# Kernel optimization log

Hardware: AMD Instinct MI355X
Metric: run time of the kernel (lower is better)

The kernel has to match this reference:

```python
import jax, jax.numpy as jnp
import numpy as np

B, T, U = 4, 200, 100
ENC_DIM = 512
PRED_DIM = 512
JOINT_DIM = 640
VOCAB = 1024


def setup_inputs() -> dict:
    key = jax.random.key(0)
    k = jax.random.split(key, 5)
    return {
        "enc_out": jax.random.normal(k[0], (B, T, ENC_DIM), dtype=jnp.float32),
        "pred_out": jax.random.normal(k[1], (B, U, PRED_DIM), dtype=jnp.float32),
        "W_enc": jax.random.normal(k[2], (ENC_DIM, JOINT_DIM), dtype=jnp.float32) / np.sqrt(ENC_DIM),
        "b_enc": jnp.zeros((JOINT_DIM,), dtype=jnp.float32),
        "W_pred": jax.random.normal(k[3], (PRED_DIM, JOINT_DIM), dtype=jnp.float32) / np.sqrt(PRED_DIM),
        "W_out": jax.random.normal(k[4], (JOINT_DIM, VOCAB), dtype=jnp.float32) / np.sqrt(JOINT_DIM),
        "b_out": jnp.zeros((VOCAB,), dtype=jnp.float32),
    }


def reference(enc_out, pred_out, W_enc, b_enc, W_pred, W_out, b_out):
    # Project encoder and prediction-net outputs to joint_dim.
    enc = jnp.einsum("bte,ej->btj", enc_out, W_enc) + b_enc      # [B,T,J]
    pred = jnp.einsum("bup,pj->buj", pred_out, W_pred)           # [B,U,J] (no bias)
    # Broadcast add -> tanh -> vocab projection.
    joint = jnp.tanh(enc[:, :, None, :] + pred[:, None, :, :])   # [B,T,U,J]
    logits = jnp.einsum("btuj,jv->btuv", joint, W_out) + b_out   # [B,T,U,V]
    return logits
```

## Files before the change

kernel.cpp:

```cpp
#include <hip/hip_runtime.h>
#include <hip/hip_bf16.h>

#define B_ 4
#define T_ 200
#define U_ 100
#define ENC_DIM 512
#define JDIM 640
#define VOCAB 1024
#define M_TOTAL (B_*T_*U_)

typedef __attribute__((ext_vector_type(8))) short short8;
typedef __attribute__((ext_vector_type(4))) float float4v;
typedef __attribute__((ext_vector_type(4))) unsigned short ushort4v;
typedef __attribute__((ext_vector_type(8))) unsigned short ushort8v;

__device__ __forceinline__ unsigned short f2bf(float x) {
    unsigned u = __builtin_bit_cast(unsigned, x);
    u += 0x7fffu + ((u >> 16) & 1u);
    return (unsigned short)(u >> 16);
}

__device__ __forceinline__ float fast_tanh(float x) {
    return 1.0f - 2.0f / (__expf(2.0f * x) + 1.0f);
}

__device__ __forceinline__ void gload_lds16(const void* g, void* l) {
    __builtin_amdgcn_global_load_lds(
        (const __attribute__((address_space(1))) unsigned int*)g,
        (__attribute__((address_space(3))) unsigned int*)l, 16, 0, 0);
}

#define PJ_BM 32
#define PJ_BN 128
#define PJ_BK 32
#define NCB   (JDIM / PJ_BN)
#define ENC_RB 25
#define PRED_RB 13
#define ENC_BLOCKS  (ENC_RB * NCB)
#define PRED_BLOCKS (PRED_RB * NCB)
#define TC_BLOCKS   (20 * 32)
#define PREP_BLOCKS (ENC_BLOCKS + PRED_BLOCKS + TC_BLOCKS)

#define XS_LD 36
#define WS_LD 132

__global__ __launch_bounds__(256)
void prep(const float* __restrict__ enc_out, const float* __restrict__ pred_out,
          const float* __restrict__ W_enc, const float* __restrict__ b_enc,
          const float* __restrict__ W_pred, const float* __restrict__ W_out,
          float* __restrict__ encp, float* __restrict__ predp,
          unsigned short* __restrict__ Wt)
{
    __shared__ float smem[PJ_BM * XS_LD + PJ_BK * WS_LD];
    const int bid = blockIdx.x;
    const int tid = threadIdx.x;

    if (bid < ENC_BLOCKS + PRED_BLOCKS) {
        const float* X; const float* W; const float* bias; float* Y; int M; int lb;
        if (bid < ENC_BLOCKS) {
            X = enc_out; W = W_enc; bias = b_enc; Y = encp; M = 800; lb = bid;
        } else {
            X = pred_out; W = W_pred; bias = nullptr; Y = predp; M = 400; lb = bid - ENC_BLOCKS;
        }
        const int row0 = (lb / NCB) * PJ_BM;
        const int col0 = (lb % NCB) * PJ_BN;

        float* Xs = smem;
        float* Ws = smem + PJ_BM * XS_LD;

        const int xr = tid >> 3;
        const int xk = (tid & 7) * 4;
        const int wrow = tid >> 5;
        const int wcol = (tid & 31) * 4;
        const int ty = tid >> 4;
        const int tx = tid & 15;

        int xrow = row0 + xr; if (xrow >= M) xrow = M - 1;

        float4v acc00 = {0,0,0,0}, acc01 = {0,0,0,0};
        float4v acc10 = {0,0,0,0}, acc11 = {0,0,0,0};

        for (int k0 = 0; k0 < ENC_DIM; k0 += PJ_BK) {
            *(float4v*)&Xs[xr * XS_LD + xk] =
                *(const float4v*)(X + (size_t)xrow * ENC_DIM + k0 + xk);
            #pragma unroll
            for (int r = 0; r < 4; ++r)
                *(float4v*)&Ws[(wrow + 8*r) * WS_LD + wcol] =
                    *(const float4v*)(W + (size_t)(k0 + wrow + 8*r) * JDIM + col0 + wcol);
            __syncthreads();
            #pragma unroll
            for (int k4 = 0; k4 < PJ_BK / 4; ++k4) {
                float4v a0 = *(const float4v*)&Xs[ty * XS_LD + k4*4];
                float4v a1 = *(const float4v*)&Xs[(ty + 16) * XS_LD + k4*4];
                #pragma unroll
                for (int q = 0; q < 4; ++q) {
                    float4v w0 = *(const float4v*)&Ws[(k4*4 + q) * WS_LD + tx*4];
                    float4v w1 = *(const float4v*)&Ws[(k4*4 + q) * WS_LD + tx*4 + 64];
                    float a0q = a0[q], a1q = a1[q];
                    acc00 += w0 * a0q;  acc01 += w1 * a0q;
                    acc10 += w0 * a1q;  acc11 += w1 * a1q;
                }
            }
            __syncthreads();
        }

        const int c0 = col0 + tx*4, c1 = c0 + 64;
        float4v bb0 = {0,0,0,0}, bb1 = {0,0,0,0};
        if (bias) { bb0 = *(const float4v*)(bias + c0); bb1 = *(const float4v*)(bias + c1); }
        int r0 = row0 + ty, r1 = row0 + ty + 16;
        if (r0 < M) {
            *(float4v*)(Y + (size_t)r0 * JDIM + c0) = acc00 + bb0;
            *(float4v*)(Y + (size_t)r0 * JDIM + c1) = acc01 + bb1;
        }
        if (r1 < M) {
            *(float4v*)(Y + (size_t)r1 * JDIM + c0) = acc10 + bb0;
            *(float4v*)(Y + (size_t)r1 * JDIM + c1) = acc11 + bb1;
        }
    } else {
        float (*tile)[33] = (float(*)[33])smem;
        const int local = bid - (ENC_BLOCKS + PRED_BLOCKS);
        const int bk = local % 20;
        const int bn = local / 20;
        const int tx = tid & 31;
        const int ty = tid >> 5;
        #pragma unroll
        for (int i = 0; i < 32; i += 8)
            tile[ty + i][tx] = W_out[(size_t)(bk * 32 + ty + i) * VOCAB + bn * 32 + tx];
        __syncthreads();
        #pragma unroll
        for (int i = 0; i < 32; i += 8)
            Wt[(size_t)(bn * 32 + ty + i) * JDIM + bk * 32 + tx] = f2bf(tile[tx][ty + i]);
    }
}

__global__ __launch_bounds__(256)
void joint_tanh(const float* __restrict__ encp, const float* __restrict__ predp,
                unsigned short* __restrict__ jbuf, int m0, int mcount) {
    int idx = blockIdx.x * 256 + threadIdx.x;
    if (idx >= mcount * (JDIM / 8)) return;
    int m  = idx / (JDIM / 8);
    int c8 = (idx - m * (JDIM / 8)) * 8;
    int mg = m0 + m;
    int b   = mg / (T_ * U_);
    int rem = mg - b * (T_ * U_);
    int t   = rem / U_;
    int u   = rem - t * U_;
    const float* eRow = encp  + (size_t)(b * T_ + t) * JDIM + c8;
    const float* pRow = predp + (size_t)(b * U_ + u) * JDIM + c8;
    float4v e0 = *(const float4v*)(eRow);
    float4v e1 = *(const float4v*)(eRow + 4);
    float4v p0 = *(const float4v*)(pRow);
    float4v p1 = *(const float4v*)(pRow + 4);
    ushort8v v;
    v.s0 = f2bf(fast_tanh(e0.x + p0.x));
    v.s1 = f2bf(fast_tanh(e0.y + p0.y));
    v.s2 = f2bf(fast_tanh(e0.z + p0.z));
    v.s3 = f2bf(fast_tanh(e0.w + p0.w));
    v.s4 = f2bf(fast_tanh(e1.x + p1.x));
    v.s5 = f2bf(fast_tanh(e1.y + p1.y));
    v.s6 = f2bf(fast_tanh(e1.z + p1.z));
    v.s7 = f2bf(fast_tanh(e1.w + p1.w));
    *(ushort8v*)(jbuf + (size_t)m * JDIM + c8) = v;
}

#define GBM 128
#define GBN 128
#define GBK 64
#define NBN (VOCAB / GBN)
#define NTILES (JDIM / GBK)

__global__ __launch_bounds__(256, 2)
void gemm_joint(const unsigned short* __restrict__ A,
                const unsigned short* __restrict__ Wt,
                const float* __restrict__ bout,
                float* __restrict__ out)
{
    __shared__ __align__(16) unsigned short As[2][GBM * GBK];
    __shared__ __align__(16) unsigned short Bs[2][GBN * GBK];

    const int tid = threadIdx.x;

    const int cpx = gridDim.x >> 3;
    const int bid = blockIdx.x;
    const int swz = (bid & 7) * cpx + (bid >> 3);
    const int bm = swz >> 3;
    const int bn = swz & (NBN - 1);

    const int srow = tid >> 3;
    const int schunk = tid & 7;
    const int scolSwz = (schunk ^ (srow & 7)) * 8;
    const unsigned short* aBase = A  + (size_t)(bm * GBM + srow) * JDIM + scolSwz;
    const unsigned short* bBase = Wt + (size_t)(bn * GBN + srow) * JDIM + scolSwz;
    const int ldsOff = tid * 8;

    const int wave = tid >> 6, lane = tid & 63;
    const int wm = (wave >> 1) * 64, wn = (wave & 1) * 64;
    const int lm = lane & 15, quad = lane >> 4;
    const int rx = lm & 7;

    float4v acc[4][4];
    #pragma unroll
    for (int i = 0; i < 4; ++i)
        #pragma unroll
        for (int j = 0; j < 4; ++j)
            acc[i][j] = (float4v){0.f, 0.f, 0.f, 0.f};

#define STAGE(buf, k0)                                                          \
    {                                                                           \
        _Pragma("unroll")                                                       \
        for (int r = 0; r < 4; ++r) {                                           \
            gload_lds16(aBase + (size_t)(r * 32) * JDIM + (k0), &As[buf][ldsOff + r * 2048]); \
            gload_lds16(bBase + (size_t)(r * 32) * JDIM + (k0), &Bs[buf][ldsOff + r * 2048]); \
        }                                                                       \
    }

#define COMPUTE(buf)                                                            \
    {                                                                           \
        _Pragma("unroll")                                                       \
        for (int kk = 0; kk < GBK; kk += 32) {                                  \
            const int cp = (((kk >> 3) + quad) ^ rx) * 8;                       \
            short8 a[4], b[4];                                                  \
            _Pragma("unroll")                                                   \
            for (int i = 0; i < 4; ++i)                                         \
                a[i] = *(const short8*)(&As[buf][(wm + i * 16 + lm) * GBK + cp]); \
            _Pragma("unroll")                                                   \
            for (int j = 0; j < 4; ++j)                                         \
                b[j] = *(const short8*)(&Bs[buf][(wn + j * 16 + lm) * GBK + cp]); \
            _Pragma("unroll")                                                   \
            for (int i = 0; i < 4; ++i)                                         \
                _Pragma("unroll")                                               \
                for (int j = 0; j < 4; ++j)                                     \
                    acc[i][j] = __builtin_amdgcn_mfma_f32_16x16x32_bf16(a[i], b[j], acc[i][j], 0, 0, 0); \
        }                                                                       \
    }

    STAGE(0, 0);
    asm volatile("s_waitcnt vmcnt(0)" ::: "memory");
    __builtin_amdgcn_s_barrier();

    int cur = 0;
    for (int t = 0; t < NTILES - 1; ++t) {
        STAGE(cur ^ 1, (t + 1) * GBK);
        COMPUTE(cur);
        asm volatile("s_waitcnt vmcnt(0)" ::: "memory");
        __builtin_amdgcn_s_barrier();
        cur ^= 1;
    }
    COMPUTE(cur);

#undef STAGE
#undef COMPUTE

    #pragma unroll
    for (int j = 0; j < 4; ++j) {
        int ng = bn * GBN + wn + j * 16 + lm;
        float bias = bout[ng];
        #pragma unroll
        for (int i = 0; i < 4; ++i) {
            int mg0 = bm * GBM + wm + i * 16 + quad * 4;
            #pragma unroll
            for (int r = 0; r < 4; ++r)
                __builtin_nontemporal_store(acc[i][j][r] + bias,
                                            out + (size_t)(mg0 + r) * VOCAB + ng);
        }
    }
}

#define BM 128
#define BN 128
#define BK 64
#define LDST 72

__global__ __launch_bounds__(256, 2)
void joint_gemm_fused(const float* __restrict__ encp, const float* __restrict__ predp,
                      const unsigned short* __restrict__ Wt, const float* __restrict__ bout,
                      float* __restrict__ out)
{
    __shared__ __align__(16) unsigned short As[BM * LDST];
    __shared__ __align__(16) unsigned short Bs[BN * LDST];
    const int tid = threadIdx.x;
    const int bm = blockIdx.x, bn = blockIdx.y;
    const int rbase = tid >> 4;
    const int c4 = (tid & 15) * 4;
    int encOff[8], predOff[8];
    #pragma unroll
    for (int i = 0; i < 8; ++i) {
        int mg  = bm * BM + i * 16 + rbase;
        int b   = mg / (T_ * U_);
        int rem = mg - b * (T_ * U_);
        int t   = rem / U_;
        int u   = rem - t * U_;
        encOff[i]  = (b * T_ + t) * JDIM + c4;
        predOff[i] = (b * U_ + u) * JDIM + c4;
    }
    const int nrow = tid >> 3;
    const int bk8  = (tid & 7) * 8;
    const size_t wtBase = (size_t)(bn * BN) * JDIM;
    const int wave = tid >> 6, lane = tid & 63;
    const int wm = (wave >> 1) * 64, wn = (wave & 1) * 64;
    const int lm = lane & 15, quad = lane >> 4;

    float4v acc[4][4];
    #pragma unroll
    for (int i = 0; i < 4; ++i)
        #pragma unroll
        for (int j = 0; j < 4; ++j)
            acc[i][j] = (float4v){0.f, 0.f, 0.f, 0.f};

    for (int k0 = 0; k0 < JDIM; k0 += BK) {
        #pragma unroll
        for (int i = 0; i < 8; ++i) {
            int row = i * 16 + rbase;
            float4v e4 = *(const float4v*)(encp + encOff[i] + k0);
            float4v p4 = *(const float4v*)(predp + predOff[i] + k0);
            ushort4v v;
            v.x = f2bf(fast_tanh(e4.x + p4.x));
            v.y = f2bf(fast_tanh(e4.y + p4.y));
            v.z = f2bf(fast_tanh(e4.z + p4.z));
            v.w = f2bf(fast_tanh(e4.w + p4.w));
            *(ushort4v*)(&As[row * LDST + c4]) = v;
        }
        #pragma unroll
        for (int i = 0; i < 4; ++i) {
            int n = i * 32 + nrow;
            float4v w = *(const float4v*)((const float*)(Wt + wtBase + (size_t)n * JDIM + k0 + bk8));
            *(float4v*)(&Bs[n * LDST + bk8]) = w;
        }
        __syncthreads();
        #pragma unroll
        for (int kk = 0; kk < BK; kk += 32) {
            short8 a[4], b[4];
            #pragma unroll
            for (int i = 0; i < 4; ++i)
                a[i] = *(const short8*)(&As[(wm + i * 16 + lm) * LDST + kk + quad * 8]);
            #pragma unroll
            for (int j = 0; j < 4; ++j)
                b[j] = *(const short8*)(&Bs[(wn + j * 16 + lm) * LDST + kk + quad * 8]);
            #pragma unroll
            for (int i = 0; i < 4; ++i)
                #pragma unroll
                for (int j = 0; j < 4; ++j)
                    acc[i][j] = __builtin_amdgcn_mfma_f32_16x16x32_bf16(a[i], b[j], acc[i][j], 0, 0, 0);
        }
        __syncthreads();
    }
    #pragma unroll
    for (int j = 0; j < 4; ++j) {
        int ng = bn * BN + wn + j * 16 + lm;
        float bias = bout[ng];
        #pragma unroll
        for (int i = 0; i < 4; ++i) {
            int mg0 = bm * BM + wm + i * 16 + quad * 4;
            #pragma unroll
            for (int r = 0; r < 4; ++r)
                out[(size_t)(mg0 + r) * VOCAB + ng] = acc[i][j][r] + bias;
        }
    }
}

extern "C" void kernel_launch(void* const* d_in, const int* in_sizes, int n_in,
                              void* d_out, int out_size, void* d_ws, size_t ws_size,
                              hipStream_t stream) {
    const float* enc_out  = (const float*)d_in[0];
    const float* pred_out = (const float*)d_in[1];
    const float* W_enc    = (const float*)d_in[2];
    const float* b_enc    = (const float*)d_in[3];
    const float* W_pred   = (const float*)d_in[4];
    const float* W_out    = (const float*)d_in[5];
    const float* b_out    = (const float*)d_in[6];
    float* out = (float*)d_out;

    float* encp  = (float*)d_ws;
    float* predp = encp + 800 * JDIM;
    unsigned short* Wt = (unsigned short*)(predp + 400 * JDIM);
    unsigned short* jbuf = Wt + (size_t)VOCAB * JDIM;

    const size_t fixedBytes = (800 * JDIM + 400 * JDIM) * sizeof(float)
                            + (size_t)VOCAB * JDIM * sizeof(unsigned short);

    prep<<<dim3(PREP_BLOCKS), 256, 0, stream>>>(enc_out, pred_out, W_enc, b_enc,
                                                W_pred, W_out, encp, predp, Wt);

    size_t avail = ws_size > fixedBytes ? ws_size - fixedBytes : 0;
    long mcMax = (long)(avail / (JDIM * sizeof(unsigned short)));
    mcMax = (mcMax / 128) * 128;
    if (mcMax > M_TOTAL) mcMax = M_TOTAL;

    if (mcMax >= 8192) {
        for (int m0 = 0; m0 < M_TOTAL; m0 += (int)mcMax) {
            int mc = M_TOTAL - m0 < mcMax ? M_TOTAL - m0 : (int)mcMax;
            int nThreads = mc * (JDIM / 8);
            joint_tanh<<<(nThreads + 255) / 256, 256, 0, stream>>>(encp, predp, jbuf, m0, mc);
            gemm_joint<<<dim3((mc / GBM) * NBN), 256, 0, stream>>>(jbuf, Wt, b_out,
                                                                   out + (size_t)m0 * VOCAB);
        }
    } else {
        joint_gemm_fused<<<dim3(M_TOTAL / BM, VOCAB / BN), 256, 0, stream>>>(encp, predp, Wt, b_out, out);
    }
}
```

Baseline: 464.3 us.

## Use 4-stage K pipeline with smaller K tile and LDS-staged coalesced epilogue

Halves the K tile to 32 and switches from double buffering to a 4-buffer ring with prefetch distance two, using partial vmcnt waits so global loads overlap more compute. A single barrier per iteration replaces the wait-then-barrier after compute. The epilogue transposes accumulators through shared memory so each thread writes contiguous float4 rows with nontemporal stores instead of scattered scalar stores. The cost is more barriers per K step and an extra LDS round-trip in the epilogue. Shared memory is sized to the epilogue buffer (about 70KB), which may reduce occupancy.

```diff
diff --git a/kernel.cpp b/kernel.cpp
--- a/kernel.cpp
+++ b/kernel.cpp
@@ -165,9 +165,10 @@
 
 #define GBM 128
 #define GBN 128
-#define GBK 64
+#define GBK 32
 #define NBN (VOCAB / GBN)
 #define NTILES (JDIM / GBK)
+#define EPI_LD 136
 
 __global__ __launch_bounds__(256, 2)
 void gemm_joint(const unsigned short* __restrict__ A,
@@ -175,8 +176,10 @@
                 const float* __restrict__ bout,
                 float* __restrict__ out)
 {
-    __shared__ __align__(16) unsigned short As[2][GBM * GBK];
-    __shared__ __align__(16) unsigned short Bs[2][GBN * GBK];
+    __shared__ __align__(16) unsigned char smem[GBN * EPI_LD * 4];
+    unsigned short* asB = (unsigned short*)smem;
+    unsigned short* bsB = asB + 4 * GBM * GBK;
+    float* epi = (float*)smem;
 
     const int tid = threadIdx.x;
 
@@ -186,9 +189,9 @@
     const int bm = swz >> 3;
     const int bn = swz & (NBN - 1);
 
-    const int srow = tid >> 3;
-    const int schunk = tid & 7;
-    const int scolSwz = (schunk ^ (srow & 7)) * 8;
+    const int srow = tid >> 2;
+    const int schunk = tid & 3;
+    const int scolSwz = (schunk ^ (srow & 3)) * 8;
     const unsigned short* aBase = A  + (size_t)(bm * GBM + srow) * JDIM + scolSwz;
     const unsigned short* bBase = Wt + (size_t)(bn * GBN + srow) * JDIM + scolSwz;
     const int ldsOff = tid * 8;
@@ -196,7 +199,12 @@
     const int wave = tid >> 6, lane = tid & 63;
     const int wm = (wave >> 1) * 64, wn = (wave & 1) * 64;
     const int lm = lane & 15, quad = lane >> 4;
-    const int rx = lm & 7;
+    const int cswz = (quad ^ (lm & 3)) * 8;
+
+    float biasj[4];
+    #pragma unroll
+    for (int j = 0; j < 4; ++j)
+        biasj[j] = bout[bn * GBN + wn + j * 16 + lm];
 
     float4v acc[4][4];
     #pragma unroll
@@ -205,63 +213,74 @@
         for (int j = 0; j < 4; ++j)
             acc[i][j] = (float4v){0.f, 0.f, 0.f, 0.f};
 
-#define STAGE(buf, k0)                                                          \
+#define STAGE(buf, t)                                                           \
     {                                                                           \
+        const int k0_ = (t) * GBK;                                              \
         _Pragma("unroll")                                                       \
-        for (int r = 0; r < 4; ++r) {                                           \
-            gload_lds16(aBase + (size_t)(r * 32) * JDIM + (k0), &As[buf][ldsOff + r * 2048]); \
-            gload_lds16(bBase + (size_t)(r * 32) * JDIM + (k0), &Bs[buf][ldsOff + r * 2048]); \
+        for (int r = 0; r < 2; ++r) {                                           \
+            gload_lds16(aBase + (size_t)(r * 64) * JDIM + k0_,                  \
+                        asB + (buf) * (GBM * GBK) + ldsOff + r * 2048);         \
+            gload_lds16(bBase + (size_t)(r * 64) * JDIM + k0_,                  \
+                        bsB + (buf) * (GBM * GBK) + ldsOff + r * 2048);         \
         }                                                                       \
     }
 
 #define COMPUTE(buf)                                                            \
     {                                                                           \
+        short8 a[4], b[4];                                                      \
         _Pragma("unroll")                                                       \
-        for (int kk = 0; kk < GBK; kk += 32) {                                  \
-            const int cp = (((kk >> 3) + quad) ^ rx) * 8;                       \
-            short8 a[4], b[4];                                                  \
-            _Pragma("unroll")                                                   \
-            for (int i = 0; i < 4; ++i)                                         \
-                a[i] = *(const short8*)(&As[buf][(wm + i * 16 + lm) * GBK + cp]); \
+        for (int i = 0; i < 4; ++i)                                             \
+            a[i] = *(const short8*)(asB + (buf) * (GBM * GBK) + (wm + i * 16 + lm) * GBK + cswz); \
+        _Pragma("unroll")                                                       \
+        for (int j = 0; j < 4; ++j)                                             \
+            b[j] = *(const short8*)(bsB + (buf) * (GBM * GBK) + (wn + j * 16 + lm) * GBK + cswz); \
+        _Pragma("unroll")                                                       \
+        for (int i = 0; i < 4; ++i)                                             \
             _Pragma("unroll")                                                   \
             for (int j = 0; j < 4; ++j)                                         \
-                b[j] = *(const short8*)(&Bs[buf][(wn + j * 16 + lm) * GBK + cp]); \
-            _Pragma("unroll")                                                   \
-            for (int i = 0; i < 4; ++i)                                         \
-                _Pragma("unroll")                                               \
-                for (int j = 0; j < 4; ++j)                                     \
-                    acc[i][j] = __builtin_amdgcn_mfma_f32_16x16x32_bf16(a[i], b[j], acc[i][j], 0, 0, 0); \
-        }                                                                       \
+                acc[i][j] = __builtin_amdgcn_mfma_f32_16x16x32_bf16(a[i], b[j], acc[i][j], 0, 0, 0); \
     }
 
     STAGE(0, 0);
-    asm volatile("s_waitcnt vmcnt(0)" ::: "memory");
-    __builtin_amdgcn_s_barrier();
-
-    int cur = 0;
-    for (int t = 0; t < NTILES - 1; ++t) {
-        STAGE(cur ^ 1, (t + 1) * GBK);
-        COMPUTE(cur);
-        asm volatile("s_waitcnt vmcnt(0)" ::: "memory");
+    STAGE(1, 1);
+
+    for (int t = 0; t < NTILES; ++t) {
+        if (t < NTILES - 1)
+            asm volatile("s_waitcnt vmcnt(4)" ::: "memory");
+        else
+            asm volatile("s_waitcnt vmcnt(0)" ::: "memory");
         __builtin_amdgcn_s_barrier();
-        cur ^= 1;
-    }
-    COMPUTE(cur);
+        if (t + 2 < NTILES)
+            STAGE((t + 2) & 3, t + 2);
+        COMPUTE(t & 3);
+    }
 
 #undef STAGE
 #undef COMPUTE
 
-    #pragma unroll
-    for (int j = 0; j < 4; ++j) {
-        int ng = bn * GBN + wn + j * 16 + lm;
-        float bias = bout[ng];
-        #pragma unroll
-        for (int i = 0; i < 4; ++i) {
-            int mg0 = bm * GBM + wm + i * 16 + quad * 4;
-            #pragma unroll
-            for (int r = 0; r < 4; ++r)
-                __builtin_nontemporal_store(acc[i][j][r] + bias,
-                                            out + (size_t)(mg0 + r) * VOCAB + ng);
+    __syncthreads();
+
+    #pragma unroll
+    for (int i = 0; i < 4; ++i)
+        #pragma unroll
+        for (int j = 0; j < 4; ++j) {
+            float4v v = acc[i][j];
+            v.x += biasj[j]; v.y += biasj[j]; v.z += biasj[j]; v.w += biasj[j];
+            *(float4v*)&epi[(wn + j * 16 + lm) * EPI_LD + wm + i * 16 + quad * 4] = v;
+        }
+
+    __syncthreads();
+
+    {
+        const int r = tid >> 1;
+        const int h = tid & 1;
+        float* dst = out + (size_t)(bm * GBM + r) * VOCAB + bn * GBN + h * 64;
+        #pragma unroll
+        for (int cc = 0; cc < 16; ++cc) {
+            const int c = h * 64 + cc * 4;
+            float4v v = { epi[(c + 0) * EPI_LD + r], epi[(c + 1) * EPI_LD + r],
+                          epi[(c + 2) * EPI_LD + r], epi[(c + 3) * EPI_LD + r] };
+            __builtin_nontemporal_store(v, (float4v*)(dst + cc * 4));
         }
     }
 }
```

After: 1.151 ms. +147.9%, slower.
